# Optimization experiments

Hardware: AMD Instinct MI355X
Metric: run time of the kernel (lower is better)

## Reference

```python
import jax, jax.numpy as jnp
import numpy as np

D_MODEL = 2048
DT_RANK = 64


def setup_inputs() -> dict:
    key = jax.random.key(0)
    ks = jax.random.split(key, 9)
    x = jax.random.normal(ks[0], (4, 2048, D_MODEL), dtype=jnp.float32)
    A = jax.random.normal(ks[1], (D_MODEL, D_MODEL), dtype=jnp.float32)
    B = jax.random.normal(ks[2], (D_MODEL, D_MODEL), dtype=jnp.float32)
    C = jax.random.normal(ks[3], (D_MODEL, D_MODEL), dtype=jnp.float32)
    Dp = jax.random.normal(ks[4], (1, D_MODEL), dtype=jnp.float32)
    # dt_project: Linear(d_model -> dt_rank); dt_project_out: Linear(dt_rank -> d_model)
    lim1 = 1.0 / np.sqrt(D_MODEL)
    W1 = jax.random.uniform(ks[5], (DT_RANK, D_MODEL), minval=-lim1, maxval=lim1, dtype=jnp.float32)
    b1 = jax.random.uniform(ks[6], (DT_RANK,), minval=-lim1, maxval=lim1, dtype=jnp.float32)
    lim2 = 1.0 / np.sqrt(DT_RANK)
    W2 = jax.random.uniform(ks[7], (D_MODEL, DT_RANK), minval=-lim2, maxval=lim2, dtype=jnp.float32)
    b2 = jax.random.uniform(ks[8], (D_MODEL,), minval=-lim2, maxval=lim2, dtype=jnp.float32)
    return {"x": x, "A": A, "B": B, "C": C, "Dp": Dp, "W1": W1, "b1": b1, "W2": W2, "b2": b2}


def reference(x, A, B, C, Dp, W1, b1, W2, b2):
    # dt = Linear_out(gelu(Linear_in(x)))  -- torch uses exact (erf) gelu
    h = jax.nn.gelu(jnp.einsum('bld,rd->blr', x, W1) + b1, approximate=False)
    dt = jnp.einsum('blr,dr->bld', h, W2) + b2
    # per-timestep loop collapses to one batched GEMM: x @ (A+B+C)
    out = jnp.einsum('bld,ds->bls', x, A + B + C)
    return out * dt + Dp  # Dp broadcasts (1, d_model)
```

## Files before the change

### kernel.cpp

```cpp
#include <hip/hip_runtime.h>
#include <stdint.h>

#define D 2048
#define R 64
#define M_TOTAL 8192

typedef float f32x4 __attribute__((ext_vector_type(4)));
typedef __bf16 bf16x8 __attribute__((ext_vector_type(8)));
typedef unsigned short u16x8 __attribute__((ext_vector_type(8)));
typedef unsigned short u16x4 __attribute__((ext_vector_type(4)));

__device__ __forceinline__ unsigned short f2bf(float f) {
  unsigned u = __builtin_bit_cast(unsigned, f);
  u += 0x7FFFu + ((u >> 16) & 1u);
  return (unsigned short)(u >> 16);
}

__device__ __forceinline__ u16x8 pack8(float4 a, float4 b) {
  u16x8 o = { f2bf(a.x), f2bf(a.y), f2bf(a.z), f2bf(a.w),
              f2bf(b.x), f2bf(b.y), f2bf(b.z), f2bf(b.w) };
  return o;
}

__device__ __forceinline__ void gload_lds16(const void* g, void* l) {
  __builtin_amdgcn_global_load_lds(
      (const __attribute__((address_space(1))) void*)g,
      (__attribute__((address_space(3))) void*)l, 16, 0, 0);
}

__global__ __launch_bounds__(512) void prep_kernel(
    const float* __restrict__ x, const float* __restrict__ A,
    const float* __restrict__ B, const float* __restrict__ C,
    const float* __restrict__ w1, const float* __restrict__ b1,
    const float* __restrict__ w2,
    unsigned short* __restrict__ xbf, unsigned short* __restrict__ st,
    unsigned short* __restrict__ w2bf, unsigned short* __restrict__ hbf) {
  __shared__ unsigned short plds[24576];
  const int t = threadIdx.x;
  const int bx = blockIdx.x;

  if (bx < 256) {
    unsigned short* sX = plds;
    unsigned short* sW = plds + 8192;
    const int m0 = bx * 32;
    const int kq = t >> 7, u = t & 127;
    const int row = u >> 2, c = u & 3;
    const int row_w = u >> 1, cw0 = (u & 1) * 2;
    const float* xp = x + (size_t)(m0 + row) * D + kq * 512 + c * 8;
    const float* wp = w1 + (size_t)row_w * D + kq * 512 + cw0 * 8;
    unsigned short* xw = xbf + (size_t)(m0 + row) * D + kq * 512 + c * 8;
    unsigned short* sXw = sX + kq * 2048 + row * 32 + (c ^ ((row >> 1) & 3)) * 8;
    const int rw2 = (row_w >> 1) & 3;
    unsigned short* sWw0 = sW + kq * 4096 + row_w * 32 + (cw0 ^ rw2) * 8;
    unsigned short* sWw1 = sW + kq * 4096 + row_w * 32 + ((cw0 + 1) ^ rw2) * 8;
    const int w = t >> 6, l = t & 63, lm = l & 15, lk = l >> 4;
    const int kqw = w >> 1, rg = w & 1;
    const int rslot = (lk ^ ((lm >> 1) & 3)) * 8;
    const unsigned short* sXr = sX + kqw * 2048 + (rg * 16 + lm) * 32 + rslot;
    const unsigned short* sWr = sW + kqw * 4096 + lm * 32 + rslot;

    f32x4 acc[4] = {};
    float4 qx[2][2], qw[2][4];
#define HLOADX(P, KT) do { qx[P][0] = *(const float4*)(xp + (KT) * 32); \
                           qx[P][1] = *(const float4*)(xp + (KT) * 32 + 4); } while (0)
#define HLOADW(P, KT) do { qw[P][0] = *(const float4*)(wp + (KT) * 32); \
                           qw[P][1] = *(const float4*)(wp + (KT) * 32 + 4); \
                           qw[P][2] = *(const float4*)(wp + (KT) * 32 + 8); \
                           qw[P][3] = *(const float4*)(wp + (KT) * 32 + 12); } while (0)
    HLOADX(0, 0); HLOADW(0, 0); HLOADX(1, 1); HLOADW(1, 1);
#define HSTEP(P, KT) do { \
    u16x8 ox = pack8(qx[P][0], qx[P][1]); \
    *(u16x8*)(sXw + (P) * 1024) = ox; \
    *(u16x8*)(xw + (KT) * 32) = ox; \
    *(u16x8*)(sWw0 + (P) * 2048) = pack8(qw[P][0], qw[P][1]); \
    *(u16x8*)(sWw1 + (P) * 2048) = pack8(qw[P][2], qw[P][3]); \
    if ((KT) + 2 < 16) { HLOADX(P, (KT) + 2); HLOADW(P, (KT) + 2); } \
    __syncthreads(); \
    { bf16x8 a_ = __builtin_bit_cast(bf16x8, *(const u16x8*)(sXr + (P) * 1024)); \
      _Pragma("unroll") \
      for (int j = 0; j < 4; ++j) { \
        bf16x8 b_ = __builtin_bit_cast(bf16x8, *(const u16x8*)(sWr + (P) * 2048 + j * 512)); \
        acc[j] = __builtin_amdgcn_mfma_f32_16x16x32_bf16(a_, b_, acc[j], 0, 0, 0); \
      } } } while (0)
#pragma unroll 1
    for (int it = 0; it < 8; ++it) { HSTEP(0, it * 2); HSTEP(1, it * 2 + 1); }
#undef HSTEP
#undef HLOADX
#undef HLOADW

    __syncthreads();
    float* red = (float*)plds;
    if (kqw > 0) {
#pragma unroll
      for (int j = 0; j < 4; ++j)
        *(f32x4*)(red + (((((kqw - 1) * 2 + rg) * 4) + j) * 64 + l) * 4) = acc[j];
    }
    __syncthreads();
    if (kqw == 0) {
      int m_base = m0 + rg * 16 + lk * 4;
#pragma unroll
      for (int j = 0; j < 4; ++j) {
        f32x4 s = acc[j];
#pragma unroll
        for (int q = 1; q < 4; ++q)
          s += *(const f32x4*)(red + (((((q - 1) * 2 + rg) * 4) + j) * 64 + l) * 4);
        int n = j * 16 + lm;
        float bv = b1[n];
#pragma unroll
        for (int r = 0; r < 4; ++r) {
          float v = s[r] + bv;
          float g = 0.5f * v * (1.0f + erff(v * 0.70710678118654752f));
          hbf[(size_t)(m_base + r) * R + n] = f2bf(g);
        }
      }
    }
  } else if (bx < 768) {
    unsigned short (*lds)[68] = (unsigned short(*)[68])plds;
    const int id = bx - 256;
    const int k0 = (id >> 5) * 128, n0 = (id & 31) * 64;
#pragma unroll
    for (int q = 0; q < 4; ++q) {
      int rowq = q * 32 + (t >> 4);
      int col = (t & 15) * 4;
      size_t off = (size_t)(k0 + rowq) * D + n0 + col;
      float4 a = *(const float4*)(A + off);
      float4 b = *(const float4*)(B + off);
      float4 cc = *(const float4*)(C + off);
      u16x4 o = { f2bf(a.x + b.x + cc.x), f2bf(a.y + b.y + cc.y),
                  f2bf(a.z + b.z + cc.z), f2bf(a.w + b.w + cc.w) };
      *(u16x4*)(&lds[rowq][col]) = o;
    }
    __syncthreads();
    const int n = t >> 3, kc = (t & 7) * 16;
    u16x8 v0, v1;
#pragma unroll
    for (int jj = 0; jj < 8; ++jj) v0[jj] = lds[kc + jj][n];
#pragma unroll
    for (int jj = 0; jj < 8; ++jj) v1[jj] = lds[kc + 8 + jj][n];
    size_t ooff = (size_t)(n0 + n) * D + k0 + kc;
    *(u16x8*)(st + ooff) = v0;
    *(u16x8*)(st + ooff + 8) = v1;
  } else {
    const int NW4 = (D * R) / 4;
    for (int i = (bx - 768) * 512 + t; i < NW4; i += 4 * 512) {
      float4 v = ((const float4*)w2)[i];
      u16x4 o = { f2bf(v.x), f2bf(v.y), f2bf(v.z), f2bf(v.w) };
      *(u16x4*)(w2bf + (size_t)i * 4) = o;
    }
  }
}

__global__ __launch_bounds__(512, 2) void gemm_kernel(
    const unsigned short* __restrict__ xbf, const unsigned short* __restrict__ st,
    const unsigned short* __restrict__ hbf, const unsigned short* __restrict__ w2bf,
    const float* __restrict__ b2, const float* __restrict__ dp,
    float* __restrict__ out) {
  __shared__ unsigned short sA[2 * 16384];
  __shared__ unsigned short sB[2 * 16384];
  const int tid = threadIdx.x;
  const int w = tid >> 6, l = tid & 63, lk = l >> 4, lm = l & 15;
  const int wm = w >> 2, wn = w & 3;
  int bid = blockIdx.x;
  int wg = (bid & 7) * 32 + (bid >> 3);
  int mb = wg >> 3, nb = wg & 7;
  int m0 = mb * 256, n0 = nb * 256;

  const int kg = (tid & 7) ^ ((tid >> 3) & 7);
  const unsigned short* gA = xbf + (size_t)(m0 + (tid >> 3)) * D + kg * 8;
  const unsigned short* gB = st + (size_t)(n0 + (tid >> 3)) * D + kg * 8;
  const int dstw = w * 512;

  const int s7 = lm & 7;
  const int gsw0 = (lk ^ s7) * 8;
  const int gsw1 = ((4 | lk) ^ s7) * 8;
  const int arow = (wm * 128 + lm) * 64;
  const int brow = (wn * 64 + lm) * 64;

  f32x4 acc[8][4] = {};

#define STAGE(gptr, sbuf, T, h) do { \
    const unsigned short* g_ = (gptr) + (size_t)((h) * 128) * D + (T) * 64; \
    unsigned short* d_ = (sbuf) + (((T) & 1) * 16384 + (h) * 8192 + dstw); \
    gload_lds16(g_, d_); \
    gload_lds16(g_ + 64 * D, d_ + 4096); } while (0)

#define LD8(buf, off) __builtin_bit_cast(bf16x8, *(const u16x8*)((buf) + (off)))

  STAGE(gA, sA, 0, 0); STAGE(gA, sA, 0, 1);
  STAGE(gB, sB, 0, 0); STAGE(gB, sB, 0, 1);
  asm volatile("s_waitcnt vmcnt(0)" ::: "memory");
  __builtin_amdgcn_s_barrier();

  const int NT = D / 64;
#pragma unroll 1
  for (int kt = 0; kt < NT; ++kt) {
    const unsigned short* bufA = sA + (kt & 1) * 16384;
    const unsigned short* bufB = sB + (kt & 1) * 16384;
    bf16x8 a[4][2], b0[2][2], b1[2][2];

    #pragma unroll
    for (int i = 0; i < 4; ++i) {
      a[i][0] = LD8(bufA, arow + i * 1024 + gsw0);
      a[i][1] = LD8(bufA, arow + i * 1024 + gsw1);
    }
    #pragma unroll
    for (int j = 0; j < 2; ++j) {
      b0[j][0] = LD8(bufB, brow + j * 1024 + gsw0);
      b0[j][1] = LD8(bufB, brow + j * 1024 + gsw1);
    }
    if (kt + 1 < NT) { STAGE(gA, sA, kt + 1, 0); STAGE(gA, sA, kt + 1, 1); }
    __builtin_amdgcn_s_barrier();
    asm volatile("s_waitcnt lgkmcnt(0)" ::: "memory");
    __builtin_amdgcn_s_setprio(1);
    #pragma unroll
    for (int i = 0; i < 4; ++i)
      #pragma unroll
      for (int j = 0; j < 2; ++j) {
        acc[i][j] = __builtin_amdgcn_mfma_f32_16x16x32_bf16(a[i][0], b0[j][0], acc[i][j], 0, 0, 0);
        acc[i][j] = __builtin_amdgcn_mfma_f32_16x16x32_bf16(a[i][1], b0[j][1], acc[i][j], 0, 0, 0);
      }
    __builtin_amdgcn_s_setprio(0);
    __builtin_amdgcn_s_barrier();

    #pragma unroll
    for (int j = 0; j < 2; ++j) {
      b1[j][0] = LD8(bufB, brow + (j + 2) * 1024 + gsw0);
      b1[j][1] = LD8(bufB, brow + (j + 2) * 1024 + gsw1);
    }
    if (kt + 1 < NT) STAGE(gB, sB, kt + 1, 0);
    __builtin_amdgcn_s_barrier();
    asm volatile("s_waitcnt lgkmcnt(0)" ::: "memory");
    __builtin_amdgcn_s_setprio(1);
    #pragma unroll
    for (int i = 0; i < 4; ++i)
      #pragma unroll
      for (int j = 0; j < 2; ++j) {
        acc[i][j + 2] = __builtin_amdgcn_mfma_f32_16x16x32_bf16(a[i][0], b1[j][0], acc[i][j + 2], 0, 0, 0);
        acc[i][j + 2] = __builtin_amdgcn_mfma_f32_16x16x32_bf16(a[i][1], b1[j][1], acc[i][j + 2], 0, 0, 0);
      }
    __builtin_amdgcn_s_setprio(0);
    __builtin_amdgcn_s_barrier();

    #pragma unroll
    for (int i = 0; i < 4; ++i) {
      a[i][0] = LD8(bufA, arow + (i + 4) * 1024 + gsw0);
      a[i][1] = LD8(bufA, arow + (i + 4) * 1024 + gsw1);
    }
    if (kt + 1 < NT) STAGE(gB, sB, kt + 1, 1);
    __builtin_amdgcn_s_barrier();
    asm volatile("s_waitcnt lgkmcnt(0)" ::: "memory");
    __builtin_amdgcn_s_setprio(1);
    #pragma unroll
    for (int i = 0; i < 4; ++i)
      #pragma unroll
      for (int j = 0; j < 2; ++j) {
        acc[i + 4][j + 2] = __builtin_amdgcn_mfma_f32_16x16x32_bf16(a[i][0], b1[j][0], acc[i + 4][j + 2], 0, 0, 0);
        acc[i + 4][j + 2] = __builtin_amdgcn_mfma_f32_16x16x32_bf16(a[i][1], b1[j][1], acc[i + 4][j + 2], 0, 0, 0);
      }
    __builtin_amdgcn_s_setprio(0);
    __builtin_amdgcn_s_barrier();

    __builtin_amdgcn_s_setprio(1);
    #pragma unroll
    for (int i = 0; i < 4; ++i)
      #pragma unroll
      for (int j = 0; j < 2; ++j) {
        acc[i + 4][j] = __builtin_amdgcn_mfma_f32_16x16x32_bf16(a[i][0], b0[j][0], acc[i + 4][j], 0, 0, 0);
        acc[i + 4][j] = __builtin_amdgcn_mfma_f32_16x16x32_bf16(a[i][1], b0[j][1], acc[i + 4][j], 0, 0, 0);
      }
    __builtin_amdgcn_s_setprio(0);
    asm volatile("s_waitcnt vmcnt(0)" ::: "memory");
    __builtin_amdgcn_s_barrier();
  }

  bf16x8 wb0[4], wb1[4];
  float b2v[4], dpv[4];
#pragma unroll
  for (int j = 0; j < 4; ++j) {
    int n = n0 + wn * 64 + j * 16 + lm;
    const u16x8* wp = (const u16x8*)(w2bf + (size_t)n * R + lk * 8);
    wb0[j] = __builtin_bit_cast(bf16x8, wp[0]);
    wb1[j] = __builtin_bit_cast(bf16x8, wp[4]);
    b2v[j] = b2[n];
    dpv[j] = dp[n];
  }
#pragma unroll
  for (int mi = 0; mi < 8; ++mi) {
    int hrow = m0 + wm * 128 + mi * 16 + lm;
    const u16x8* hp = (const u16x8*)(hbf + (size_t)hrow * R + lk * 8);
    bf16x8 ha0 = __builtin_bit_cast(bf16x8, hp[0]);
    bf16x8 ha1 = __builtin_bit_cast(bf16x8, hp[4]);
    int mbase = m0 + wm * 128 + mi * 16 + lk * 4;
#pragma unroll
    for (int j = 0; j < 4; ++j) {
      f32x4 dt = {};
      dt = __builtin_amdgcn_mfma_f32_16x16x32_bf16(ha0, wb0[j], dt, 0, 0, 0);
      dt = __builtin_amdgcn_mfma_f32_16x16x32_bf16(ha1, wb1[j], dt, 0, 0, 0);
      int n = n0 + wn * 64 + j * 16 + lm;
#pragma unroll
      for (int r = 0; r < 4; ++r) {
        float val = acc[mi][j][r] * (dt[r] + b2v[j]) + dpv[j];
        out[(size_t)(mbase + r) * D + n] = val;
      }
    }
  }
#undef STAGE
#undef LD8
}

extern "C" void kernel_launch(void* const* d_in, const int* in_sizes, int n_in,
                              void* d_out, int out_size, void* d_ws, size_t ws_size,
                              hipStream_t stream) {
  const float* x  = (const float*)d_in[0];
  const float* A  = (const float*)d_in[1];
  const float* B  = (const float*)d_in[2];
  const float* C  = (const float*)d_in[3];
  const float* Dp = (const float*)d_in[4];
  const float* W1 = (const float*)d_in[5];
  const float* b1 = (const float*)d_in[6];
  const float* W2 = (const float*)d_in[7];
  const float* b2 = (const float*)d_in[8];
  float* out = (float*)d_out;

  uint8_t* ws = (uint8_t*)d_ws;
  unsigned short* xbf  = (unsigned short*)ws;
  unsigned short* st   = (unsigned short*)(ws + (32u << 20));
  unsigned short* w2bf = (unsigned short*)(ws + (40u << 20));
  unsigned short* hbf  = (unsigned short*)(ws + (41u << 20));

  prep_kernel<<<772, 512, 0, stream>>>(x, A, B, C, W1, b1, W2, xbf, st, w2bf, hbf);
  gemm_kernel<<<256, 512, 0, stream>>>(xbf, st, hbf, w2bf, b2, Dp, out);
}
```

Before: 100.2 us.

## Deepen GEMM global prefetch to two tiles and cut per-iteration barriers

The main loop now keeps two K-tiles of global-to-LDS loads in flight. Tiles 0 and 1 are issued in the prologue. Each iteration issues the loads for tile kt+2 into the buffer it has just finished reading, then waits with vmcnt(8) so that only the next tile must be resident. The B second-half LDS reads are hoisted ahead of the first MFMA block, the barriers drop from five per iteration to two, and sched_barrier fences pin the instruction order. This aims to hide global load latency and barrier stalls better. The cost is relying on exact vmcnt accounting and on the reuse of the current buffer only after every wave has finished its LDS reads.

```diff
diff --git a/kernel.cpp b/kernel.cpp
--- a/kernel.cpp
+++ b/kernel.cpp
@@ -185,15 +185,19 @@
     gload_lds16(g_ + 64 * D, d_ + 4096); } while (0)
 
 #define LD8(buf, off) __builtin_bit_cast(bf16x8, *(const u16x8*)((buf) + (off)))
+#define SB0() __builtin_amdgcn_sched_barrier(0)
 
   STAGE(gA, sA, 0, 0); STAGE(gA, sA, 0, 1);
   STAGE(gB, sB, 0, 0); STAGE(gB, sB, 0, 1);
-  asm volatile("s_waitcnt vmcnt(0)" ::: "memory");
+  STAGE(gA, sA, 1, 0); STAGE(gA, sA, 1, 1);
+  STAGE(gB, sB, 1, 0); STAGE(gB, sB, 1, 1);
+  asm volatile("s_waitcnt vmcnt(8)" ::: "memory");
   __builtin_amdgcn_s_barrier();
 
   const int NT = D / 64;
 #pragma unroll 1
   for (int kt = 0; kt < NT; ++kt) {
+    SB0();
     const unsigned short* bufA = sA + (kt & 1) * 16384;
     const unsigned short* bufB = sB + (kt & 1) * 16384;
     bf16x8 a[4][2], b0[2][2], b1[2][2];
@@ -208,9 +212,14 @@
       b0[j][0] = LD8(bufB, brow + j * 1024 + gsw0);
       b0[j][1] = LD8(bufB, brow + j * 1024 + gsw1);
     }
-    if (kt + 1 < NT) { STAGE(gA, sA, kt + 1, 0); STAGE(gA, sA, kt + 1, 1); }
-    __builtin_amdgcn_s_barrier();
     asm volatile("s_waitcnt lgkmcnt(0)" ::: "memory");
+    SB0();
+    #pragma unroll
+    for (int j = 0; j < 2; ++j) {
+      b1[j][0] = LD8(bufB, brow + (j + 2) * 1024 + gsw0);
+      b1[j][1] = LD8(bufB, brow + (j + 2) * 1024 + gsw1);
+    }
+    SB0();
     __builtin_amdgcn_s_setprio(1);
     #pragma unroll
     for (int i = 0; i < 4; ++i)
@@ -220,16 +229,9 @@
         acc[i][j] = __builtin_amdgcn_mfma_f32_16x16x32_bf16(a[i][1], b0[j][1], acc[i][j], 0, 0, 0);
       }
     __builtin_amdgcn_s_setprio(0);
-    __builtin_amdgcn_s_barrier();
-
-    #pragma unroll
-    for (int j = 0; j < 2; ++j) {
-      b1[j][0] = LD8(bufB, brow + (j + 2) * 1024 + gsw0);
-      b1[j][1] = LD8(bufB, brow + (j + 2) * 1024 + gsw1);
-    }
-    if (kt + 1 < NT) STAGE(gB, sB, kt + 1, 0);
-    __builtin_amdgcn_s_barrier();
+
     asm volatile("s_waitcnt lgkmcnt(0)" ::: "memory");
+    SB0();
     __builtin_amdgcn_s_setprio(1);
     #pragma unroll
     for (int i = 0; i < 4; ++i)
@@ -239,16 +241,22 @@
         acc[i][j + 2] = __builtin_amdgcn_mfma_f32_16x16x32_bf16(a[i][1], b1[j][1], acc[i][j + 2], 0, 0, 0);
       }
     __builtin_amdgcn_s_setprio(0);
-    __builtin_amdgcn_s_barrier();
-
+    SB0();
     #pragma unroll
     for (int i = 0; i < 4; ++i) {
       a[i][0] = LD8(bufA, arow + (i + 4) * 1024 + gsw0);
       a[i][1] = LD8(bufA, arow + (i + 4) * 1024 + gsw1);
     }
-    if (kt + 1 < NT) STAGE(gB, sB, kt + 1, 1);
+
+    asm volatile("s_waitcnt lgkmcnt(0)" ::: "memory");
+    SB0();
     __builtin_amdgcn_s_barrier();
-    asm volatile("s_waitcnt lgkmcnt(0)" ::: "memory");
+    SB0();
+    if (kt + 2 < NT) {
+      STAGE(gA, sA, kt + 2, 0); STAGE(gA, sA, kt + 2, 1);
+      STAGE(gB, sB, kt + 2, 0); STAGE(gB, sB, kt + 2, 1);
+    }
+    SB0();
     __builtin_amdgcn_s_setprio(1);
     #pragma unroll
     for (int i = 0; i < 4; ++i)
@@ -257,10 +265,6 @@
         acc[i + 4][j + 2] = __builtin_amdgcn_mfma_f32_16x16x32_bf16(a[i][0], b1[j][0], acc[i + 4][j + 2], 0, 0, 0);
         acc[i + 4][j + 2] = __builtin_amdgcn_mfma_f32_16x16x32_bf16(a[i][1], b1[j][1], acc[i + 4][j + 2], 0, 0, 0);
       }
-    __builtin_amdgcn_s_setprio(0);
-    __builtin_amdgcn_s_barrier();
-
-    __builtin_amdgcn_s_setprio(1);
     #pragma unroll
     for (int i = 0; i < 4; ++i)
       #pragma unroll
@@ -269,7 +273,9 @@
         acc[i + 4][j] = __builtin_amdgcn_mfma_f32_16x16x32_bf16(a[i][1], b0[j][1], acc[i + 4][j], 0, 0, 0);
       }
     __builtin_amdgcn_s_setprio(0);
-    asm volatile("s_waitcnt vmcnt(0)" ::: "memory");
+    if (kt < NT - 2) asm volatile("s_waitcnt vmcnt(8)" ::: "memory");
+    else             asm volatile("s_waitcnt vmcnt(0)" ::: "memory");
+    SB0();
     __builtin_amdgcn_s_barrier();
   }
 
@@ -306,6 +312,7 @@
   }
 #undef STAGE
 #undef LD8
+#undef SB0
 }
 
 extern "C" void kernel_launch(void* const* d_in, const int* in_sizes, int n_in,
```

After: 105.2 us. 5.0% more time.

## Deepen GEMM pipeline to prefetch two tiles ahead with split waitcnts

Applied to the files above, without the earlier changes.

Restructures the bf16 MFMA main loop so global-to-LDS staging runs two k-tiles ahead instead of one, with the loop unrolled by two over alternating LDS buffers. LDS fragment reads for the next tile's A(0-3) and B(0-1) are issued inside the current tile, and partial lgkmcnt/vmcnt waits plus sched_barriers replace the full waits. The aim is to hide global-load and LDS latency behind MFMA work and stop draining every queue each iteration. The risk is more live registers and subtle buffer-reuse hazards, since a stage is overwritten while earlier reads may still be in flight.

```diff
diff --git a/kernel.cpp b/kernel.cpp
--- a/kernel.cpp
+++ b/kernel.cpp
@@ -176,101 +176,89 @@
   const int arow = (wm * 128 + lm) * 64;
   const int brow = (wn * 64 + lm) * 64;
 
+  const int NT = D / 64;
   f32x4 acc[8][4] = {};
-
-#define STAGE(gptr, sbuf, T, h) do { \
+  bf16x8 aA[4][2], aB[4][2], bt[2][2], be[2][2], bo[2][2];
+
+#define BUFA(S) (sA + (S) * 16384)
+#define BUFB(S) (sB + (S) * 16384)
+#define LD8(buf, off) __builtin_bit_cast(bf16x8, *(const u16x8*)((buf) + (off)))
+#define SB0() __builtin_amdgcn_sched_barrier(0)
+#define BAR() __builtin_amdgcn_s_barrier()
+#define LGKM4() asm volatile("s_waitcnt lgkmcnt(4)" ::: "memory")
+#define LGKM8() asm volatile("s_waitcnt lgkmcnt(8)" ::: "memory")
+
+#define STAGE2(gptr, sbuf, T, h, S) do { if ((T) < NT) { \
     const unsigned short* g_ = (gptr) + (size_t)((h) * 128) * D + (T) * 64; \
-    unsigned short* d_ = (sbuf) + (((T) & 1) * 16384 + (h) * 8192 + dstw); \
+    unsigned short* d_ = (sbuf) + ((S) * 16384 + (h) * 8192 + dstw); \
     gload_lds16(g_, d_); \
-    gload_lds16(g_ + 64 * D, d_ + 4096); } while (0)
-
-#define LD8(buf, off) __builtin_bit_cast(bf16x8, *(const u16x8*)((buf) + (off)))
-
-  STAGE(gA, sA, 0, 0); STAGE(gA, sA, 0, 1);
-  STAGE(gB, sB, 0, 0); STAGE(gB, sB, 0, 1);
-  asm volatile("s_waitcnt vmcnt(0)" ::: "memory");
-  __builtin_amdgcn_s_barrier();
-
-  const int NT = D / 64;
+    gload_lds16(g_ + 64 * D, d_ + 4096); } } while (0)
+
+#define RD_A03(S) do { _Pragma("unroll") for (int i = 0; i < 4; ++i) { \
+    aA[i][0] = LD8(BUFA(S), arow + i * 1024 + gsw0); \
+    aA[i][1] = LD8(BUFA(S), arow + i * 1024 + gsw1); } } while (0)
+#define RD_A47(S) do { _Pragma("unroll") for (int i = 0; i < 4; ++i) { \
+    aB[i][0] = LD8(BUFA(S), arow + (i + 4) * 1024 + gsw0); \
+    aB[i][1] = LD8(BUFA(S), arow + (i + 4) * 1024 + gsw1); } } while (0)
+#define RD_B23(S) do { _Pragma("unroll") for (int j = 0; j < 2; ++j) { \
+    bt[j][0] = LD8(BUFB(S), brow + (j + 2) * 1024 + gsw0); \
+    bt[j][1] = LD8(BUFB(S), brow + (j + 2) * 1024 + gsw1); } } while (0)
+#define RD_B01(S, DST) do { _Pragma("unroll") for (int j = 0; j < 2; ++j) { \
+    DST[j][0] = LD8(BUFB(S), brow + j * 1024 + gsw0); \
+    DST[j][1] = LD8(BUFB(S), brow + j * 1024 + gsw1); } } while (0)
+
+#define QUAD(AR, BR, IO, JO) do { \
+    __builtin_amdgcn_s_setprio(1); \
+    _Pragma("unroll") for (int i = 0; i < 4; ++i) \
+    _Pragma("unroll") for (int j = 0; j < 2; ++j) { \
+      acc[i + IO][j + JO] = __builtin_amdgcn_mfma_f32_16x16x32_bf16(AR[i][0], BR[j][0], acc[i + IO][j + JO], 0, 0, 0); \
+      acc[i + IO][j + JO] = __builtin_amdgcn_mfma_f32_16x16x32_bf16(AR[i][1], BR[j][1], acc[i + IO][j + JO], 0, 0, 0); \
+    } \
+    __builtin_amdgcn_s_setprio(0); } while (0)
+
+#define TILE(S, BCUR, BNXT, KT) do { \
+     \
+    RD_B23(S); \
+    STAGE2(gB, sB, (KT) + 2, 0, S); \
+    SB0(); BAR(); LGKM4(); SB0(); \
+    QUAD(aA, BCUR, 0, 0); \
+    SB0(); BAR(); \
+     \
+    RD_A47(S); \
+    STAGE2(gA, sA, (KT) + 2, 0, S); \
+    SB0(); BAR(); LGKM8(); SB0(); \
+    QUAD(aA, bt, 0, 2); \
+    SB0(); BAR(); \
+     \
+    RD_A03((S) ^ 1); \
+    STAGE2(gB, sB, (KT) + 2, 1, S); \
+    SB0(); BAR(); LGKM8(); SB0(); \
+    QUAD(aB, bt, 4, 2); \
+    SB0(); BAR(); \
+     \
+    RD_B01((S) ^ 1, BNXT); \
+    STAGE2(gA, sA, (KT) + 2, 1, S); \
+    if ((KT) < NT - 2) asm volatile("s_waitcnt vmcnt(4)" ::: "memory"); \
+    else               asm volatile("s_waitcnt vmcnt(0)" ::: "memory"); \
+    SB0(); BAR(); LGKM4(); SB0(); \
+    QUAD(aB, BCUR, 4, 0); \
+    SB0(); BAR(); } while (0)
+
+  STAGE2(gB, sB, 0, 0, 0); STAGE2(gA, sA, 0, 0, 0);
+  STAGE2(gB, sB, 0, 1, 0); STAGE2(gA, sA, 0, 1, 0);
+  STAGE2(gB, sB, 1, 0, 1); STAGE2(gA, sA, 1, 0, 1);
+  STAGE2(gB, sB, 1, 1, 1); STAGE2(gA, sA, 1, 1, 1);
+  asm volatile("s_waitcnt vmcnt(2)" ::: "memory");
+  BAR();
+  RD_A03(0);
+  RD_B01(0, be);
+  SB0();
+
 #pragma unroll 1
-  for (int kt = 0; kt < NT; ++kt) {
-    const unsigned short* bufA = sA + (kt & 1) * 16384;
-    const unsigned short* bufB = sB + (kt & 1) * 16384;
-    bf16x8 a[4][2], b0[2][2], b1[2][2];
-
-    #pragma unroll
-    for (int i = 0; i < 4; ++i) {
-      a[i][0] = LD8(bufA, arow + i * 1024 + gsw0);
-      a[i][1] = LD8(bufA, arow + i * 1024 + gsw1);
-    }
-    #pragma unroll
-    for (int j = 0; j < 2; ++j) {
-      b0[j][0] = LD8(bufB, brow + j * 1024 + gsw0);
-      b0[j][1] = LD8(bufB, brow + j * 1024 + gsw1);
-    }
-    if (kt + 1 < NT) { STAGE(gA, sA, kt + 1, 0); STAGE(gA, sA, kt + 1, 1); }
-    __builtin_amdgcn_s_barrier();
-    asm volatile("s_waitcnt lgkmcnt(0)" ::: "memory");
-    __builtin_amdgcn_s_setprio(1);
-    #pragma unroll
-    for (int i = 0; i < 4; ++i)
-      #pragma unroll
-      for (int j = 0; j < 2; ++j) {
-        acc[i][j] = __builtin_amdgcn_mfma_f32_16x16x32_bf16(a[i][0], b0[j][0], acc[i][j], 0, 0, 0);
-        acc[i][j] = __builtin_amdgcn_mfma_f32_16x16x32_bf16(a[i][1], b0[j][1], acc[i][j], 0, 0, 0);
-      }
-    __builtin_amdgcn_s_setprio(0);
-    __builtin_amdgcn_s_barrier();
-
-    #pragma unroll
-    for (int j = 0; j < 2; ++j) {
-      b1[j][0] = LD8(bufB, brow + (j + 2) * 1024 + gsw0);
-      b1[j][1] = LD8(bufB, brow + (j + 2) * 1024 + gsw1);
-    }
-    if (kt + 1 < NT) STAGE(gB, sB, kt + 1, 0);
-    __builtin_amdgcn_s_barrier();
-    asm volatile("s_waitcnt lgkmcnt(0)" ::: "memory");
-    __builtin_amdgcn_s_setprio(1);
-    #pragma unroll
-    for (int i = 0; i < 4; ++i)
-      #pragma unroll
-      for (int j = 0; j < 2; ++j) {
-        acc[i][j + 2] = __builtin_amdgcn_mfma_f32_16x16x32_bf16(a[i][0], b1[j][0], acc[i][j + 2], 0, 0, 0);
-        acc[i][j + 2] = __builtin_amdgcn_mfma_f32_16x16x32_bf16(a[i][1], b1[j][1], acc[i][j + 2], 0, 0, 0);
-      }
-    __builtin_amdgcn_s_setprio(0);
-    __builtin_amdgcn_s_barrier();
-
-    #pragma unroll
-    for (int i = 0; i < 4; ++i) {
-      a[i][0] = LD8(bufA, arow + (i + 4) * 1024 + gsw0);
-      a[i][1] = LD8(bufA, arow + (i + 4) * 1024 + gsw1);
-    }
-    if (kt + 1 < NT) STAGE(gB, sB, kt + 1, 1);
-    __builtin_amdgcn_s_barrier();
-    asm volatile("s_waitcnt lgkmcnt(0)" ::: "memory");
-    __builtin_amdgcn_s_setprio(1);
-    #pragma unroll
-    for (int i = 0; i < 4; ++i)
-      #pragma unroll
-      for (int j = 0; j < 2; ++j) {
-        acc[i + 4][j + 2] = __builtin_amdgcn_mfma_f32_16x16x32_bf16(a[i][0], b1[j][0], acc[i + 4][j + 2], 0, 0, 0);
-        acc[i + 4][j + 2] = __builtin_amdgcn_mfma_f32_16x16x32_bf16(a[i][1], b1[j][1], acc[i + 4][j + 2], 0, 0, 0);
-      }
-    __builtin_amdgcn_s_setprio(0);
-    __builtin_amdgcn_s_barrier();
-
-    __builtin_amdgcn_s_setprio(1);
-    #pragma unroll
-    for (int i = 0; i < 4; ++i)
-      #pragma unroll
-      for (int j = 0; j < 2; ++j) {
-        acc[i + 4][j] = __builtin_amdgcn_mfma_f32_16x16x32_bf16(a[i][0], b0[j][0], acc[i + 4][j], 0, 0, 0);
-        acc[i + 4][j] = __builtin_amdgcn_mfma_f32_16x16x32_bf16(a[i][1], b0[j][1], acc[i + 4][j], 0, 0, 0);
-      }
-    __builtin_amdgcn_s_setprio(0);
-    asm volatile("s_waitcnt vmcnt(0)" ::: "memory");
-    __builtin_amdgcn_s_barrier();
+  for (int it = 0; it < NT / 2; ++it) {
+    const int kt0 = it * 2;
+    TILE(0, be, bo, kt0);
+    TILE(1, bo, be, kt0 + 1);
   }
 
   bf16x8 wb0[4], wb1[4];
@@ -304,8 +292,20 @@
       }
     }
   }
-#undef STAGE
+#undef TILE
+#undef QUAD
+#undef RD_A03
+#undef RD_A47
+#undef RD_B23
+#undef RD_B01
+#undef STAGE2
+#undef LGKM4
+#undef LGKM8
+#undef BAR
+#undef SB0
 #undef LD8
+#undef BUFA
+#undef BUFB
 }
 
 extern "C" void kernel_launch(void* const* d_in, const int* in_sizes, int n_in,
```

Result: no change. 99.27 us (-0.9%).
